# Performance work log

Hardware: AMD Instinct MI355X
Metric: run time of the kernel (lower is better)

Reference implementation:

```python
import jax, jax.numpy as jnp
import numpy as np
from jax import lax

PAD = 2
M1 = M2 = 12

def _gelu(v):
    return jax.nn.gelu(v, approximate=False)

def _spectral_conv(h, w1, w2):
    # h: [B,C,H,W] real; w1,w2: [C,C,M1,M2] complex64
    B, C, H, W = h.shape
    Wf = W // 2 + 1
    hft = jnp.fft.rfft2(h)  # [B,C,H,Wf] complex
    top = jnp.einsum('bixy,ioxy->boxy', hft[:, :, :M1, :M2], w1)
    bot = jnp.einsum('bixy,ioxy->boxy', hft[:, :, -M1:, :M2], w2)
    out_ft = jnp.zeros((B, C, H, Wf), jnp.complex64)
    out_ft = out_ft.at[:, :, :M1, :M2].set(top)
    out_ft = out_ft.at[:, :, -M1:, :M2].set(bot)
    return jnp.fft.irfft2(out_ft, s=(H, W))

def reference(x, grid, sentence_embeddings, fc0_w, fc0_b, sc_w1, sc_w2, wc_w, wc_b,
              pe1_w, pe1_b, pe2_w, pe2_b,
              sp_w1, sp_b1, sp_w2, sp_b2, sp_w3, sp_b3,
              xp_w1, xp_b1, xp_w2, xp_b2, xp_w3, xp_b3,
              pu_w1, pu_b1, pu_w2, pu_b2, pu_w3, pu_b3,
              fc1_w, fc1_b, fc2_w, fc2_b):
    B = x.shape[0]
    # sentence projection: Linear-ReLU-Linear-ReLU-Linear
    s = jax.nn.relu(sentence_embeddings @ sp_w1 + sp_b1)
    s = jax.nn.relu(s @ sp_w2 + sp_b2)
    sentence_emb = s @ sp_w3 + sp_b3  # [B,16]

    h = jnp.concatenate([x, grid], axis=-1) @ fc0_w + fc0_b  # [B,32,32,C]
    h = h.transpose(0, 3, 1, 2)  # [B,C,32,32]
    h = jnp.pad(h, ((0, 0), (0, 0), (0, PAD), (0, PAD)))  # [B,C,34,34]

    for i in range(4):
        w1 = sc_w1[i, ..., 0] + 1j * sc_w1[i, ..., 1]
        w2 = sc_w2[i, ..., 0] + 1j * sc_w2[i, ..., 1]
        x1 = _spectral_conv(h, w1, w2)
        x2 = jnp.einsum('bchw,oc->bohw', h, wc_w[i]) + wc_b[i][None, :, None, None]
        h = x1 + x2
        if i < 3:
            h = _gelu(h)  # dropout = identity (eval mode)

    # PatchEmbed: conv(k=8,s=4) -> gelu -> 1x1 conv
    p = lax.conv_general_dilated(h, pe1_w, (4, 4), 'VALID',
                                 dimension_numbers=('NCHW', 'OIHW', 'NCHW'))
    p = _gelu(p + pe1_b[None, :, None, None])  # [B,1,7,7]
    p = jnp.einsum('bchw,oc->bohw', p, pe2_w) + pe2_b[None, :, None, None]
    p = p.reshape(B, -1)  # [B,49]

    e = jax.nn.silu(p @ xp_w1 + xp_b1)
    e = jax.nn.silu(e @ xp_w2 + xp_b2)
    x_emb = e @ xp_w3 + xp_b3  # [B,16]

    emb = jnp.concatenate([x_emb, sentence_emb], axis=-1)  # [B,32]
    emb = jax.nn.silu(emb @ pu_w1 + pu_b1)
    emb = jax.nn.silu(emb @ pu_w2 + pu_b2)
    emb = (emb @ pu_w3 + pu_b3).reshape(B, 1, 34, 34)

    h = jnp.concatenate([h, emb], axis=1)  # [B,C+1,34,34]
    h = h[..., :-PAD, :-PAD]  # [B,C+1,32,32]
    h = h.transpose(0, 2, 3, 1)
    h = _gelu(h @ fc1_w + fc1_b)
    out = h @ fc2_w + fc2_b
    return out[..., None, :]  # [B,32,32,1,num_channels]

def setup_inputs() -> dict:
    key = jax.random.key(0)
    ks = iter(jax.random.split(key, 64))
    def rn(shape, scale=1.0):
        return jax.random.normal(next(ks), shape, jnp.float32) * scale
    C = 64
    inp = {
        'x': rn((256, 32, 32, 40)),
        'grid': jax.random.uniform(next(ks), (256, 32, 32, 2), jnp.float32),
        'sentence_embeddings': rn((256, 384)),
        'fc0_w': rn((42, C), 42 ** -0.5), 'fc0_b': jnp.zeros((C,), jnp.float32),
        'sc_w1': rn((4, C, C, M1, M2, 2), 1.0 / (C * C)),
        'sc_w2': rn((4, C, C, M1, M2, 2), 1.0 / (C * C)),
        'wc_w': rn((4, C, C), C ** -0.5), 'wc_b': jnp.zeros((4, C), jnp.float32),
        'pe1_w': rn((1, C, 8, 8), (C * 64) ** -0.5), 'pe1_b': jnp.zeros((1,), jnp.float32),
        'pe2_w': rn((1, 1)), 'pe2_b': jnp.zeros((1,), jnp.float32),
        'sp_w1': rn((384, 32), 384 ** -0.5), 'sp_b1': jnp.zeros((32,), jnp.float32),
        'sp_w2': rn((32, 32), 32 ** -0.5), 'sp_b2': jnp.zeros((32,), jnp.float32),
        'sp_w3': rn((32, 16), 32 ** -0.5), 'sp_b3': jnp.zeros((16,), jnp.float32),
        'xp_w1': rn((49, 32), 49 ** -0.5), 'xp_b1': jnp.zeros((32,), jnp.float32),
        'xp_w2': rn((32, 32), 32 ** -0.5), 'xp_b2': jnp.zeros((32,), jnp.float32),
        'xp_w3': rn((32, 16), 32 ** -0.5), 'xp_b3': jnp.zeros((16,), jnp.float32),
        'pu_w1': rn((32, 128), 32 ** -0.5), 'pu_b1': jnp.zeros((128,), jnp.float32),
        'pu_w2': rn((128, 256), 128 ** -0.5), 'pu_b2': jnp.zeros((256,), jnp.float32),
        'pu_w3': rn((256, 1156), 256 ** -0.5), 'pu_b3': jnp.zeros((1156,), jnp.float32),
        'fc1_w': rn((C + 1, 128), (C + 1) ** -0.5), 'fc1_b': jnp.zeros((128,), jnp.float32),
        'fc2_w': rn((128, 4), 128 ** -0.5), 'fc2_b': jnp.zeros((4,), jnp.float32),
    }
    return inp
```

## Files before the change

kernel.cpp:

```cpp
#include <hip/hip_runtime.h>
#include <hip/hip_bf16.h>
#include <math.h>

typedef __hip_bfloat16 bf16;
typedef __bf16 bfv8 __attribute__((ext_vector_type(8)));
typedef float fv4 __attribute__((ext_vector_type(4)));

__device__ __forceinline__ float bff(const bf16 x){ return __bfloat162float(x); }
__device__ __forceinline__ float gelu_f(float v){
    float x = v * 0.70710678118654752f;
    float ax = fabsf(x);
    float t = __builtin_amdgcn_rcpf(1.0f + 0.3275911f * ax);
    float y = t*(0.254829592f + t*(-0.284496736f + t*(1.421413741f +
              t*(-1.453152027f + t*1.061405429f))));
    float er = 1.0f - y * __expf(-ax*ax);
    er = (x < 0.f) ? -er : er;
    return 0.5f * v * (1.0f + er);
}
__device__ __forceinline__ float silu_f(float v){
    return v / (1.f + __expf(-v));
}
__device__ __forceinline__ float rdf(const void* p, size_t i, bool f32){
    return f32 ? ((const float*)p)[i] : __bfloat162float(((const bf16*)p)[i]);
}
__device__ __forceinline__ unsigned int packbf2(float a, float b){
    __hip_bfloat162 v;
    v.x = __float2bfloat16(a);
    v.y = __float2bfloat16(b);
    return *reinterpret_cast<unsigned int*>(&v);
}
__device__ __forceinline__ float2 unpackbf2(unsigned int u){
    __hip_bfloat162 v = *reinterpret_cast<__hip_bfloat162*>(&u);
    return make_float2(__bfloat162float(v.x), __bfloat162float(v.y));
}
__device__ __forceinline__ float us2f(unsigned short u){
    unsigned int x = ((unsigned int)u) << 16;
    return __uint_as_float(x);
}
__device__ __forceinline__ unsigned short f2us(float f){
    bf16 v = __float2bfloat16(f);
    return *reinterpret_cast<unsigned short*>(&v);
}


__global__ __launch_bounds__(256) void k_probe(const void* x, float* flag){
    __shared__ int wild;
    int t = threadIdx.x;
    if (t == 0) wild = 0;
    __syncthreads();
    const bf16* xb = (const bf16*)x;
    for (int i = t; i < 1024; i += 256){
        float v = bff(xb[i]);
        if (!(fabsf(v) < 1e10f)) wild = 1;
    }
    __syncthreads();
    if (t == 0) flag[0] = wild ? 1.f : 0.f;
}

__global__ __launch_bounds__(256) void k_tables(float* tabs, float* fwdimg,
                                                const void* __restrict__ fc0w,
                                                const void* __restrict__ fc0b,
                                                const float* __restrict__ flg){
    int t = threadIdx.x;
    const bool f32 = (flg[0] > 0.5f);
    unsigned int* gBT = (unsigned int*)(tabs + 2448);
    unsigned int* gW2 = (unsigned int*)(tabs + 3536);
    unsigned short* gB1 = (unsigned short*)fwdimg;
    unsigned short* gB2 = (unsigned short*)(fwdimg + 1024);
    unsigned short* gF  = (unsigned short*)(fwdimg + 3328);
    float* gFb = fwdimg + 5632;
    const float TWO_PI = 6.283185307179586f;
    for (int i = t; i < 4608; i += 256){
        int c = i / 72, k = i - c*72;
        float v = (k < 42) ? rdf(fc0w, (size_t)k*64 + c, f32) : 0.f;
        gF[i] = f2us(v);
    }
    if (t < 64) gFb[t] = rdf(fc0b, t, f32);
    for (int i = t; i < 2048; i += 256){
        int row = i >> 6, k = i & 63;
        float v = 0.f;
        if (row < 24 && k < 34){
            int kx = row >> 1, s = row & 1;
            int ph = (kx * k) % 34;
            float ang = TWO_PI * (float)ph / 34.0f;
            float sn, cs;
            sincosf(ang, &sn, &cs);
            v = (s == 0) ? cs : -sn;
        }
        gB1[i] = f2us(v);
    }
    for (int i = t; i < 4608; i += 256){
        int row = i / 96, kk = i - row*96;
        float v = 0.f;
        if (kk < 68){
            int kyi = row >> 1, s = row & 1;
            int y = kk >> 1, p = kk & 1;
            int ky = (kyi < 12) ? kyi : kyi + 10;
            int ph = (ky * y) % 34;
            float ang = TWO_PI * (float)ph / 34.0f;
            float sn, cs;
            sincosf(ang, &sn, &cs);
            float wr = cs, wi = -sn;
            v = (s == 0) ? ((p == 0) ? wr : -wi) : ((p == 0) ? wi : wr);
        }
        gB2[i] = f2us(v);
    }
    for (int i = t; i < 1088; i += 256){
        int n = i >> 4, kd = i & 15;
        int x = n >> 1, ri = n & 1;
        int kx = kd;
        float v0 = 0.f, v1 = 0.f;
        if (kx < 12){
            int ph = (kx * x) % 34;
            float ang = TWO_PI * (float)ph / 34.0f;
            float s, c;
            sincosf(ang, &s, &c);
            float ck = (kx == 0) ? 1.0f : 2.0f;
            float C = ck * c, S = ck * s;
            v0 = (ri == 0) ? C : S;
            v1 = (ri == 0) ? -S : C;
        }
        gBT[i] = packbf2(v0, v1);
    }
    for (int i = t; i < 1088; i += 256){
        int y = i >> 5, kd = i & 31;
        int kyi = kd;
        float v0 = 0.f, v1 = 0.f;
        if (kyi < 24){
            int ky = (kyi < 12) ? kyi : kyi + 10;
            int ph = (ky * y) % 34;
            float ang = TWO_PI * (float)ph / 34.0f;
            float s, c;
            sincosf(ang, &s, &c);
            v0 = c * (1.0f/1156.0f);
            v1 = -s * (1.0f/1156.0f);
        }
        gW2[i] = packbf2(v0, v1);
    }
}

__global__ __launch_bounds__(256) void k_fc0(const void* __restrict__ xin,
                                             const void* __restrict__ grd,
                                             const unsigned short* __restrict__ img,
                                             bf16* __restrict__ h,
                                             const float* __restrict__ flg){
    __shared__ unsigned short sA[128*72];
    const bool f32 = (flg[0] > 0.5f);
    int B = blockIdx.x;
    int b = (B >> 6)*8 + (B & 7);
    int u = (B >> 3) & 7;
    int t = threadIdx.x;
    unsigned int* sAw = (unsigned int*)sA;
    if (!f32){
        const unsigned int* xd = (const unsigned int*)xin;
        size_t base = ((size_t)b*1024 + u*128)*20;
        for (int i = t; i < 2560; i += 256){
            int p = i / 20, kd = i - p*20;
            sAw[p*36 + kd] = xd[base + i];
        }
        const unsigned int* gd = (const unsigned int*)grd;
        size_t gb = (size_t)b*1024 + (size_t)u*128;
        if (t < 128) sAw[t*36 + 20] = gd[gb + t];
    } else {
        const float* xf = (const float*)xin;
        size_t base = ((size_t)b*1024 + u*128)*40;
        for (int i = t; i < 2560; i += 256){
            int p = i / 20, kd = i - p*20;
            sAw[p*36 + kd] = packbf2(xf[base + 2*i], xf[base + 2*i + 1]);
        }
        const float* gf = (const float*)grd;
        size_t gb = ((size_t)b*1024 + u*128)*2;
        if (t < 128) sAw[t*36 + 20] = packbf2(gf[gb + 2*t], gf[gb + 2*t + 1]);
    }
    for (int i = t; i < 1920; i += 256){
        int p = i / 15, j = i - p*15;
        sAw[p*36 + 21 + j] = 0;
    }
    __syncthreads();
    int ln = t & 15, qd = (t & 63) >> 4, wv = t >> 6;
    const float* gbias = (const float*)(img + 4608);
    bfv8 bfr[4][2];
    #pragma unroll
    for (int nt = 0; nt < 4; ++nt)
        #pragma unroll
        for (int ks = 0; ks < 2; ++ks)
            bfr[nt][ks] = *reinterpret_cast<const bfv8*>(&img[(nt*16 + ln)*72 + ks*32 + qd*8]);
    bfv8 a_[2][2];
    #pragma unroll
    for (int mi = 0; mi < 2; ++mi){
        int mt = wv*2 + mi;
        a_[mi][0] = *reinterpret_cast<const bfv8*>(&sA[(mt*16 + ln)*72 + qd*8]);
        a_[mi][1] = *reinterpret_cast<const bfv8*>(&sA[(mt*16 + ln)*72 + 32 + qd*8]);
    }
    fv4 acc[2][4];
    #pragma unroll
    for (int mi = 0; mi < 2; ++mi)
        #pragma unroll
        for (int nt = 0; nt < 4; ++nt){
            fv4 a = (fv4){0.f,0.f,0.f,0.f};
            a = __builtin_amdgcn_mfma_f32_16x16x32_bf16(a_[mi][0], bfr[nt][0], a, 0, 0, 0);
            a = __builtin_amdgcn_mfma_f32_16x16x32_bf16(a_[mi][1], bfr[nt][1], a, 0, 0, 0);
            acc[mi][nt] = a;
        }
    __syncthreads();
    unsigned int* sCd = (unsigned int*)sA;
    {
        int c = t >> 2, r = t & 3;
        sCd[c*68 + r*17 + 16] = 0;
    }
    #pragma unroll
    for (int mi = 0; mi < 2; ++mi)
        #pragma unroll
        for (int nt = 0; nt < 4; ++nt){
            int c = nt*16 + ln;
            float bb = gbias[c];
            int pl = (wv*2 + mi)*16 + qd*4;
            int y = pl >> 5, x = pl & 31;
            int di = c*68 + y*17 + (x >> 1);
            sCd[di]     = packbf2(acc[mi][nt][0] + bb, acc[mi][nt][1] + bb);
            sCd[di + 1] = packbf2(acc[mi][nt][2] + bb, acc[mi][nt][3] + bb);
        }
    __syncthreads();
    unsigned int* hw = (unsigned int*)(h + (size_t)b*73984);
    for (int i = t; i < 4352; i += 256){
        int c = i / 68, d = i - c*68;
        hw[c*578 + u*68 + d] = sCd[i];
    }
    if (u == 7){
        for (int i = t; i < 2176; i += 256){
            int c = i / 34, d = i - c*34;
            hw[c*578 + 544 + d] = 0;
        }
    }
}

__global__ __launch_bounds__(256) void k_fwd(const bf16* __restrict__ h,
                                             unsigned int* __restrict__ hft,
                                             const unsigned short* __restrict__ fwdimg){
    __shared__ unsigned short lds[15360];
    unsigned short* sA1 = lds;
    unsigned short* sA2 = lds + 10368;
    unsigned int* sA1w = (unsigned int*)sA1;
    unsigned int* sA2w = (unsigned int*)sA2;
    const unsigned short* gB1 = fwdimg;
    const unsigned short* gB2 = fwdimg + 2048;
    int blk = blockIdx.x;
    int b = blk >> 4, c0 = (blk & 15) * 4;
    int t = threadIdx.x;
    const unsigned int* srcp = (const unsigned int*)(h + (size_t)b*73984 + (size_t)c0*1156);
    for (int i = t; i < 2312; i += 256){
        int c = i / 578; int rem = i - c*578;
        int y = rem / 17; int d = rem - y*17;
        sA1w[(c*34 + y)*36 + d] = srcp[i];
    }
    for (int i = t; i < 2040; i += 256){
        int r = i / 15, d = i - r*15;
        sA1w[r*36 + 17 + d] = 0;
    }
    for (int i = t; i < 288; i += 256){
        int r = 136 + i / 36, d = i - (i/36)*36;
        sA1w[r*36 + d] = 0;
    }
    for (int i = t; i < 672; i += 256){
        int r = i / 14, d = i - r*14;
        sA2w[r*52 + 34 + d] = 0;
    }
    __syncthreads();
    int ln = t & 15, qd = (t & 63) >> 4, wv = t >> 6;
    {
        int ntw = wv & 1;
        bfv8 b1f[2];
        #pragma unroll
        for (int ks = 0; ks < 2; ++ks)
            b1f[ks] = *reinterpret_cast<const bfv8*>(&gB1[(ntw*16 + ln)*64 + ks*32 + qd*8]);
        int col = ntw*16 + ln;
        int kx = col >> 1, s = col & 1;
        for (int mt = (wv >> 1); mt < 9; mt += 2){
            fv4 acc = (fv4){0.f,0.f,0.f,0.f};
            #pragma unroll
            for (int ks = 0; ks < 2; ++ks){
                bfv8 a = *reinterpret_cast<const bfv8*>(&sA1[(mt*16 + ln)*72 + ks*32 + qd*8]);
                acc = __builtin_amdgcn_mfma_f32_16x16x32_bf16(a, b1f[ks], acc, 0, 0, 0);
            }
            if (col < 24){
                #pragma unroll
                for (int rr = 0; rr < 4; ++rr){
                    int r = mt*16 + qd*4 + rr;
                    if (r < 136){
                        int c = r / 34, y = r - c*34;
                        sA2[(c*12 + kx)*104 + 2*y + s] = f2us(acc[rr]);
                    }
                }
            }
        }
    }
    __syncthreads();
    unsigned short* sC = sA1;
    for (int tau = wv; tau < 9; tau += 4){
        int mt = tau / 3, nt = tau - (tau/3)*3;
        fv4 acc = (fv4){0.f,0.f,0.f,0.f};
        #pragma unroll
        for (int ks = 0; ks < 3; ++ks){
            bfv8 a  = *reinterpret_cast<const bfv8*>(&sA2[(mt*16 + ln)*104 + ks*32 + qd*8]);
            bfv8 bb = *reinterpret_cast<const bfv8*>(&gB2[(nt*16 + ln)*96 + ks*32 + qd*8]);
            acc = __builtin_amdgcn_mfma_f32_16x16x32_bf16(a, bb, acc, 0, 0, 0);
        }
        int col = nt*16 + ln;
        int ky = col >> 1, s = col & 1;
        #pragma unroll
        for (int rr = 0; rr < 4; ++rr){
            int r = mt*16 + qd*4 + rr;
            int c = r / 12, kxx = r - c*12;
            sC[(ky*12 + kxx)*9 + s*4 + c] = f2us(acc[rr]);
        }
    }
    __syncthreads();
    unsigned int* dst = hft + ((size_t)(c0 >> 2)*256 + b)*1152;
    for (int d = t; d < 1152; d += 256){
        int m = d >> 2, j = d & 3;
        unsigned int lo = sC[m*9 + 2*j];
        unsigned int hi = sC[m*9 + 2*j + 1];
        dst[d] = lo | (hi << 16);
    }
}

__global__ __launch_bounds__(256) void k_mixm(const unsigned short* __restrict__ hft,
                                              const void* __restrict__ sc_w1,
                                              const void* __restrict__ sc_w2,
                                              unsigned int* __restrict__ mixed, int layer,
                                              const float* __restrict__ flg){
    __shared__ unsigned short sB[128*136];
    const bool f32 = (flg[0] > 0.5f);
    int B = blockIdx.x;
    int x8 = B & 7, w8 = B >> 3;
    int r4 = w8 & 3, g = w8 >> 2;
    int u = g*8 + x8;
    int mh = u & 1;
    int m  = (u >> 1)*4 + r4;
    int b0 = mh * 128;
    int t = threadIdx.x;
    int kyi = m / 12, kx = m - kyi*12;
    const void* w = (kyi < 12) ? sc_w1 : sc_w2;
    int r = (kyi < 12) ? kyi : kyi - 12;
    size_t wbase = (size_t)layer * 64*64*144*2;
    for (int idx = t; idx < 4096; idx += 256){
        int i = idx >> 6, o = idx & 63;
        size_t off = wbase + (((size_t)idx*12 + r)*12 + kx)*2;
        float wr = rdf(w, off, f32);
        float wi = rdf(w, off+1, f32);
        int kre = ((i >> 2) << 3) + (i & 3);
        sB[o*136 + kre]          = f2us(wr);
        sB[(o+64)*136 + kre]     = f2us(wi);
        sB[o*136 + kre + 4]      = f2us(-wi);
        sB[(o+64)*136 + kre + 4] = f2us(wr);
    }
    __syncthreads();
    int ln = t & 15, qd = (t & 63) >> 4, wv = t >> 6;
    bfv8 af[2][4];
    int arow = b0 + wv*32 + ln;
    #pragma unroll
    for (int tm = 0; tm < 2; ++tm)
        #pragma unroll
        for (int ks = 0; ks < 4; ++ks){
            int gg = ks*4 + qd;
            af[tm][ks] = *reinterpret_cast<const bfv8*>(
                hft + (((size_t)gg*256 + arow + tm*16)*288 + m)*8);
        }
    fv4 acc[2][8];
    #pragma unroll
    for (int tm=0;tm<2;++tm)
        #pragma unroll
        for (int tn=0;tn<8;++tn) acc[tm][tn] = (fv4){0.f,0.f,0.f,0.f};
    #pragma unroll
    for (int ks = 0; ks < 4; ++ks){
        bfv8 bfr[8];
        #pragma unroll
        for (int tn = 0; tn < 8; ++tn)
            bfr[tn] = *reinterpret_cast<const bfv8*>(&sB[(tn*16 + ln)*136 + ks*32 + qd*8]);
        #pragma unroll
        for (int tm = 0; tm < 2; ++tm)
            #pragma unroll
            for (int tn = 0; tn < 8; ++tn)
                acc[tm][tn] = __builtin_amdgcn_mfma_f32_16x16x32_bf16(af[tm][ks], bfr[tn], acc[tm][tn], 0, 0, 0);
    }
    __syncthreads();
    #pragma unroll
    for (int tm = 0; tm < 2; ++tm)
        #pragma unroll
        for (int tn = 0; tn < 8; ++tn)
            #pragma unroll
            for (int rr = 0; rr < 4; ++rr){
                int row = wv*32 + tm*16 + qd*4 + rr;
                int col = tn*16 + ln;
                sB[row*136 + col] = f2us(acc[tm][tn][rr]);
            }
    __syncthreads();
    for (int idx = t; idx < 8192; idx += 256){
        int row = idx >> 6, o = idx & 63;
        unsigned int pr = ((unsigned int)sB[row*136 + o]) |
                          (((unsigned int)sB[row*136 + o + 64]) << 16);
        mixed[((size_t)(b0 + row)*288 + m)*64 + o] = pr;
    }
}

__global__ __launch_bounds__(256) void k_wc(bf16* __restrict__ h,
                                            const void* __restrict__ wc_w,
                                            const void* __restrict__ wc_b,
                                            int layer,
                                            const float* __restrict__ flg){
    __shared__ unsigned short sA[240*72];
    __shared__ unsigned short sBT[64*72];
    __shared__ float sb[64];
    const bool f32 = (flg[0] > 0.5f);
    int blk = blockIdx.x;
    int b = blk & 255, u = blk >> 8;
    int px0 = u*240;
    int npx = 1156 - px0; if (npx > 240) npx = 240;
    int ndp = npx >> 1;
    int t = threadIdx.x;
    size_t wbase = (size_t)layer*4096;
    for (int i = t; i < 4096; i += 256){
        int o = i >> 6, c = i & 63;
        sBT[o*72 + c] = f2us(rdf(wc_w, wbase + i, f32));
    }
    if (t < 64) sb[t] = rdf(wc_b, layer*64 + t, f32);
    const unsigned int* srcd = (const unsigned int*)(h + (size_t)b*73984);
    for (int i = t; i < 7680; i += 256){
        int c = i / 120, dp = i - c*120;
        unsigned int v = (dp < ndp) ? srcd[c*578 + (px0 >> 1) + dp] : 0u;
        sA[(2*dp)*72 + c]     = (unsigned short)(v & 0xffff);
        sA[(2*dp + 1)*72 + c] = (unsigned short)(v >> 16);
    }
    __syncthreads();
    int ln = t & 15, qd = (t & 63) >> 4, wv = t >> 6;
    bfv8 bfr[4][2];
    #pragma unroll
    for (int nt = 0; nt < 4; ++nt)
        #pragma unroll
        for (int ks = 0; ks < 2; ++ks)
            bfr[nt][ks] = *reinterpret_cast<const bfv8*>(&sBT[(nt*16 + ln)*72 + ks*32 + qd*8]);
    bfv8 a_[4][2];
    #pragma unroll
    for (int mi = 0; mi < 4; ++mi){
        int mt = wv + mi*4;
        if (mt < 15){
            a_[mi][0] = *reinterpret_cast<const bfv8*>(&sA[(mt*16 + ln)*72 + qd*8]);
            a_[mi][1] = *reinterpret_cast<const bfv8*>(&sA[(mt*16 + ln)*72 + 32 + qd*8]);
        }
    }
    fv4 acc[4][4];
    #pragma unroll
    for (int mi = 0; mi < 4; ++mi){
        int mt = wv + mi*4;
        if (mt < 15){
            #pragma unroll
            for (int nt = 0; nt < 4; ++nt){
                fv4 a = (fv4){0.f,0.f,0.f,0.f};
                a = __builtin_amdgcn_mfma_f32_16x16x32_bf16(a_[mi][0], bfr[nt][0], a, 0, 0, 0);
                a = __builtin_amdgcn_mfma_f32_16x16x32_bf16(a_[mi][1], bfr[nt][1], a, 0, 0, 0);
                acc[mi][nt] = a;
            }
        }
    }
    __syncthreads();
    unsigned int* sCd = (unsigned int*)sA;
    #pragma unroll
    for (int mi = 0; mi < 4; ++mi){
        int mt = wv + mi*4;
        if (mt < 15){
            #pragma unroll
            for (int nt = 0; nt < 4; ++nt){
                int o = nt*16 + ln;
                float bb = sb[o];
                int p0 = mt*16 + qd*4;
                sCd[o*120 + (p0 >> 1)]     = packbf2(acc[mi][nt][0] + bb, acc[mi][nt][1] + bb);
                sCd[o*120 + (p0 >> 1) + 1] = packbf2(acc[mi][nt][2] + bb, acc[mi][nt][3] + bb);
            }
        }
    }
    __syncthreads();
    unsigned int* dstd = (unsigned int*)(h + (size_t)b*73984);
    for (int i = t; i < 7680; i += 256){
        int o = i / 120, dp = i - o*120;
        if (dp < ndp) dstd[o*578 + (px0 >> 1) + dp] = sCd[o*120 + dp];
    }
}

__global__ __launch_bounds__(256, 5) void k_invm(const unsigned int* __restrict__ mixed,
                                              const float* __restrict__ tabs,
                                              bf16* __restrict__ hio, int layer){
    __shared__ unsigned short lds[15072];
    unsigned short* sA   = lds;
    unsigned short* sG16 = lds + 3840;
    unsigned int* ldsw   = (unsigned int*)lds;
    unsigned int* sGd    = ldsw + 1920;
    float* rawf          = (float*)(ldsw + 1920);
    int B = blockIdx.x;
    int x8 = B & 7, s4 = (B >> 3) & 3, z = B >> 5;
    int b  = (z >> 2)*8 + x8;
    int o0 = ((z & 3)*4 + s4)*4;
    int t = threadIdx.x;
    const unsigned short* gBT16 = (const unsigned short*)(tabs + 2448);
    const unsigned short* gW216 = (const unsigned short*)(tabs + 3536);
    const unsigned int* msrc = mixed + (size_t)b*18432 + o0;
    for (int i = t; i < 1152; i += 256){
        int m = i >> 2, ch = i & 3;
        int kyi = m / 12, kx = m - kyi*12;
        ((unsigned int*)sA)[(ch*24 + kyi)*20 + kx] = msrc[(size_t)m*64 + ch];
    }
    for (int i = t; i < 384; i += 256)
        ((unsigned int*)sA)[(i >> 2)*20 + 12 + (i & 3)] = 0;
    for (int i = t; i < 1088; i += 256){
        int r = i >> 3;
        int ch = r / 34, x = r - ch*34;
        sGd[(ch*36 + x)*36 + 24 + (i & 7)] = 0;
    }
    __syncthreads();
    int ln = t & 15, qd = (t & 63) >> 4, wv = t >> 6;
    for (int tau = wv; tau < 30; tau += 4){
        int mt = tau / 5, nt = tau - mt*5;
        bfv8 a  = *reinterpret_cast<const bfv8*>(&sA[(mt*16 + ln)*40 + qd*8]);
        bfv8 bb = *reinterpret_cast<const bfv8*>(&gBT16[(nt*16 + ln)*32 + qd*8]);
        fv4 acc = (fv4){0.f,0.f,0.f,0.f};
        acc = __builtin_amdgcn_mfma_f32_16x16x32_bf16(a, bb, acc, 0, 0, 0);
        int col = nt*16 + ln;
        if (col < 68){
            int x = col >> 1, ri = col & 1;
            #pragma unroll
            for (int rr = 0; rr < 4; ++rr){
                int row = mt*16 + qd*4 + rr;
                int ch = row / 24, kyi = row - ch*24;
                sG16[(ch*36 + x)*72 + 2*kyi + ri] = f2us(acc[rr]);
            }
        }
    }
    __syncthreads();
    int ch = wv;
    fv4 accB[3][3];
    #pragma unroll
    for (int mt = 0; mt < 3; ++mt){
        bfv8 a0 = *reinterpret_cast<const bfv8*>(&gW216[(mt*16 + ln)*64 + qd*8]);
        bfv8 a1 = *reinterpret_cast<const bfv8*>(&gW216[(mt*16 + ln)*64 + 32 + qd*8]);
        #pragma unroll
        for (int nt = 0; nt < 3; ++nt){
            bfv8 b0 = *reinterpret_cast<const bfv8*>(&sG16[(ch*36 + nt*16 + ln)*72 + qd*8]);
            bfv8 b1 = *reinterpret_cast<const bfv8*>(&sG16[(ch*36 + nt*16 + ln)*72 + 32 + qd*8]);
            fv4 acc = (fv4){0.f,0.f,0.f,0.f};
            acc = __builtin_amdgcn_mfma_f32_16x16x32_bf16(a0, b0, acc, 0, 0, 0);
            acc = __builtin_amdgcn_mfma_f32_16x16x32_bf16(a1, b1, acc, 0, 0, 0);
            accB[mt][nt] = acc;
        }
    }
    __syncthreads();
    #pragma unroll
    for (int mt = 0; mt < 3; ++mt)
        #pragma unroll
        for (int nt = 0; nt < 3; ++nt){
            int x = nt*16 + ln;
            if (x < 34){
                #pragma unroll
                for (int rr = 0; rr < 4; ++rr){
                    int y = mt*16 + qd*4 + rr;
                    if (y < 34) rawf[ch*1156 + y*34 + x] = accB[mt][nt][rr];
                }
            }
        }
    __syncthreads();
    const unsigned int* hsrc = (const unsigned int*)(hio + (size_t)b*73984 + (size_t)o0*1156);
    unsigned int* hdst = (unsigned int*)(hio + (size_t)b*73984 + (size_t)o0*1156);
    for (int i = t; i < 2312; i += 256){
        float2 rv = *reinterpret_cast<const float2*>(&rawf[2*i]);
        float2 hv = unpackbf2(hsrc[i]);
        float v0 = rv.x + hv.x, v1 = rv.y + hv.y;
        if (layer < 3){ v0 = gelu_f(v0); v1 = gelu_f(v1); }
        hdst[i] = packbf2(v0, v1);
    }
}

__global__ __launch_bounds__(256) void k_pe(const bf16* __restrict__ h,
                                            const void* __restrict__ pw,
                                            const void* __restrict__ pb,
                                            const void* __restrict__ p2w,
                                            const void* __restrict__ p2b,
                                            float* __restrict__ p49,
                                            const float* __restrict__ flg){
    __shared__ float red[256];
    const bool f32 = (flg[0] > 0.5f);
    int bid = blockIdx.x;
    int b = bid / 49, r = bid - b*49;
    int py = r / 7, px = r - py*7;
    int t = threadIdx.x;
    const bf16* hb = h + (size_t)b*73984 + (py*4)*34 + px*4;
    float partial = 0.f;
    for (int tt = t; tt < 4096; tt += 256){
        int c = tt >> 6, k = tt & 63, ky = k >> 3, kx = k & 7;
        partial += bff(hb[(size_t)c*1156 + ky*34 + kx]) * rdf(pw, tt, f32);
    }
    red[t] = partial;
    __syncthreads();
    for (int s = 128; s > 0; s >>= 1){
        if (t < s) red[t] += red[t + s];
        __syncthreads();
    }
    if (t == 0){
        float v = red[0] + rdf(pb, 0, f32);
        v = gelu_f(v);
        p49[bid] = v * rdf(p2w, 0, f32) + rdf(p2b, 0, f32);
    }
}

__global__ __launch_bounds__(256) void k_sent(const void* __restrict__ se,
                                             const void* __restrict__ w1, const void* __restrict__ b1,
                                             const void* __restrict__ w2, const void* __restrict__ b2,
                                             const void* __restrict__ w3, const void* __restrict__ b3,
                                             float* __restrict__ outv,
                                             const float* __restrict__ flg){
    __shared__ float sse[384];
    __shared__ float red[256];
    __shared__ float s1[32], s2[32];
    const bool f32 = (flg[0] > 0.5f);
    int b = blockIdx.x, t = threadIdx.x;
    for (int i = t; i < 384; i += 256) sse[i] = rdf(se, (size_t)b*384 + i, f32);
    __syncthreads();
    {
        int o = t & 31, g = t >> 5;
        float acc = 0.f;
        #pragma unroll 4
        for (int k = g*48; k < g*48 + 48; ++k)
            acc += sse[k] * rdf(w1, (size_t)k*32 + o, f32);
        red[t] = acc;
    }
    __syncthreads();
    if (t < 32){
        float a = rdf(b1, t, f32);
        #pragma unroll
        for (int g = 0; g < 8; ++g) a += red[g*32 + t];
        s1[t] = fmaxf(a, 0.f);
    }
    __syncthreads();
    if (t < 32){
        float acc = rdf(b2, t, f32);
        for (int k = 0; k < 32; ++k) acc += s1[k] * rdf(w2, k*32 + t, f32);
        s2[t] = fmaxf(acc, 0.f);
    }
    __syncthreads();
    if (t < 16){
        float acc = rdf(b3, t, f32);
        for (int k = 0; k < 32; ++k) acc += s2[k] * rdf(w3, k*16 + t, f32);
        outv[b*16 + t] = acc;
    }
}

__global__ __launch_bounds__(256) void k_xp(const float* __restrict__ p49,
                                           const void* __restrict__ w1, const void* __restrict__ b1,
                                           const void* __restrict__ w2, const void* __restrict__ b2,
                                           const void* __restrict__ w3, const void* __restrict__ b3,
                                           float* __restrict__ outv,
                                           const float* __restrict__ flg){
    __shared__ float sp[49];
    __shared__ float red[256];
    __shared__ float s1[32], s2[32];
    const bool f32 = (flg[0] > 0.5f);
    int b = blockIdx.x, t = threadIdx.x;
    if (t < 49) sp[t] = p49[b*49 + t];
    __syncthreads();
    {
        int o = t & 31, g = t >> 5;
        float acc = 0.f;
        for (int k = g; k < 49; k += 8)
            acc += sp[k] * rdf(w1, (size_t)k*32 + o, f32);
        red[t] = acc;
    }
    __syncthreads();
    if (t < 32){
        float a = rdf(b1, t, f32);
        #pragma unroll
        for (int g = 0; g < 8; ++g) a += red[g*32 + t];
        s1[t] = silu_f(a);
    }
    __syncthreads();
    if (t < 32){
        float acc = rdf(b2, t, f32);
        for (int k = 0; k < 32; ++k) acc += s1[k] * rdf(w2, k*32 + t, f32);
        s2[t] = silu_f(acc);
    }
    __syncthreads();
    if (t < 16){
        float acc = rdf(b3, t, f32);
        for (int k = 0; k < 32; ++k) acc += s2[k] * rdf(w3, k*16 + t, f32);
        outv[b*16 + t] = acc;
    }
}

__global__ __launch_bounds__(256) void k_puA(const float* __restrict__ xemb,
                                             const float* __restrict__ semb,
                                             const void* __restrict__ w1, const void* __restrict__ b1,
                                             const void* __restrict__ w2, const void* __restrict__ b2,
                                             float* __restrict__ h2buf,
                                             const float* __restrict__ flg){
    __shared__ float ein[32];
    __shared__ float h1[128];
    const bool f32 = (flg[0] > 0.5f);
    int b = blockIdx.x, t = threadIdx.x;
    if (t < 16) ein[t] = xemb[b*16 + t];
    else if (t < 32) ein[t] = semb[b*16 + (t - 16)];
    __syncthreads();
    if (t < 128){
        float acc = rdf(b1, t, f32);
        for (int k = 0; k < 32; ++k) acc += ein[k] * rdf(w1, k*128 + t, f32);
        h1[t] = silu_f(acc);
    }
    __syncthreads();
    {
        float acc = rdf(b2, t, f32);
        for (int k = 0; k < 128; ++k) acc += h1[k] * rdf(w2, k*256 + t, f32);
        h2buf[(size_t)b*256 + t] = silu_f(acc);
    }
}

__global__ __launch_bounds__(256) void k_puB(const float* __restrict__ h2buf,
                                             const void* __restrict__ w3, const void* __restrict__ b3,
                                             float* __restrict__ emb,
                                             const float* __restrict__ flg){
    __shared__ float sh2[256];
    const bool f32 = (flg[0] > 0.5f);
    int blk = blockIdx.x;
    int b = blk & 255, nc = blk >> 8;
    int t = threadIdx.x;
    sh2[t] = h2buf[(size_t)b*256 + t];
    __syncthreads();
    int e = nc*232 + t;
    if (t < 232 && e < 1156){
        float acc = rdf(b3, e, f32);
        if (f32){
            const float* wp = (const float*)w3 + e;
            #pragma unroll 4
            for (int k = 0; k < 256; ++k) acc += sh2[k] * wp[(size_t)k*1156];
        } else {
            const bf16* wp = (const bf16*)w3 + e;
            #pragma unroll 4
            for (int k = 0; k < 256; ++k) acc += sh2[k] * bff(wp[(size_t)k*1156]);
        }
        emb[(size_t)b*1156 + e] = acc;
    }
}

__global__ __launch_bounds__(256, 3) void k_final(const bf16* __restrict__ h,
                                                  const float* __restrict__ emb,
                                                  const void* __restrict__ w1, const void* __restrict__ b1,
                                                  const void* __restrict__ w2, const void* __restrict__ b2,
                                                  void* __restrict__ out,
                                                  const float* __restrict__ flg){
    __shared__ unsigned short sw1t[128*72];
    __shared__ unsigned short sw2t[16*136];
    __shared__ float sw1e[128];
    __shared__ float sb1[128];
    __shared__ float sb2[4];
    __shared__ unsigned short spx[64*66];
    __shared__ float sembp[64];
    __shared__ unsigned short sh2[128*66];
    const bool f32 = (flg[0] > 0.5f);
    int blk = blockIdx.x;
    int b = blk >> 1, half = blk & 1;
    int t = threadIdx.x;
    for (int i = t; i < 8320; i += 256){
        int c = i >> 7, j = i & 127;
        float v = rdf(w1, i, f32);
        if (c < 64) sw1t[j*72 + c] = f2us(v);
        else sw1e[j] = v;
    }
    if (t < 128) sb1[t] = rdf(b1, t, f32);
    for (int i = t; i < 2176; i += 256){
        int n = i / 136, j = i - n*136;
        float v = (n < 4 && j < 128) ? rdf(w2, j*4 + n, f32) : 0.f;
        sw2t[i] = f2us(v);
    }
    if (t < 4) sb2[t] = rdf(b2, t, f32);
    __syncthreads();
    int ln = t & 15, qd = (t & 63) >> 4, wv = t >> 6;
    bfv8 bw1[8][2];
    #pragma unroll
    for (int tn = 0; tn < 8; ++tn)
        #pragma unroll
        for (int ks = 0; ks < 2; ++ks)
            bw1[tn][ks] = *reinterpret_cast<const bfv8*>(&sw1t[(tn*16 + ln)*72 + ks*32 + qd*8]);
    bfv8 bw2[4];
    #pragma unroll
    for (int ks = 0; ks < 4; ++ks)
        bw2[ks] = *reinterpret_cast<const bfv8*>(&sw2t[ln*136 + ks*32 + qd*8]);
    const bf16* hb = h + (size_t)b*73984;
    const float* eb = emb + (size_t)b*1156;
    for (int it = 0; it < 8; ++it){
        int y0 = half*16 + it*2;
        __syncthreads();
        for (int e = t; e < 2048; e += 256){
            int c = e >> 5, d = e & 31;
            int px = d*2;
            int y = y0 + (px >> 5), x = px & 31;
            float v0 = bff(hb[(size_t)c*1156 + y*34 + x]);
            int px1 = px + 1;
            int y1 = y0 + (px1 >> 5), x1 = px1 & 31;
            float v1 = bff(hb[(size_t)c*1156 + y1*34 + x1]);
            ((unsigned int*)spx)[c*33 + d] = packbf2(v0, v1);
        }
        if (t < 64){
            int y = y0 + (t >> 5), x = t & 31;
            sembp[t] = eb[y*34 + x];
        }
        __syncthreads();
        fv4 acc[8];
        #pragma unroll
        for (int tn = 0; tn < 8; ++tn) acc[tn] = (fv4){0.f,0.f,0.f,0.f};
        #pragma unroll
        for (int ks = 0; ks < 2; ++ks){
            union { bfv8 v; unsigned short s[8]; } af;
            #pragma unroll
            for (int j = 0; j < 8; ++j)
                af.s[j] = spx[(ks*32 + qd*8 + j)*66 + wv*16 + ln];
            #pragma unroll
            for (int tn = 0; tn < 8; ++tn)
                acc[tn] = __builtin_amdgcn_mfma_f32_16x16x32_bf16(af.v, bw1[tn][ks], acc[tn], 0, 0, 0);
        }
        float ev[4];
        #pragma unroll
        for (int rr = 0; rr < 4; ++rr) ev[rr] = sembp[wv*16 + qd*4 + rr];
        #pragma unroll
        for (int tn = 0; tn < 8; ++tn){
            int col = tn*16 + ln;
            float we = sw1e[col];
            float bb1 = sb1[col];
            #pragma unroll
            for (int rr = 0; rr < 4; ++rr){
                float v = acc[tn][rr] + ev[rr]*we + bb1;
                sh2[col*66 + wv*16 + qd*4 + rr] = f2us(gelu_f(v));
            }
        }
        __syncthreads();
        fv4 a2 = (fv4){0.f,0.f,0.f,0.f};
        #pragma unroll
        for (int ks = 0; ks < 4; ++ks){
            union { bfv8 v; unsigned short s[8]; } af;
            #pragma unroll
            for (int j = 0; j < 8; ++j)
                af.s[j] = sh2[(ks*32 + qd*8 + j)*66 + wv*16 + ln];
            a2 = __builtin_amdgcn_mfma_f32_16x16x32_bf16(af.v, bw2[ks], a2, 0, 0, 0);
        }
        if (ln < 4){
            float bb2 = sb2[ln];
            #pragma unroll
            for (int rr = 0; rr < 4; ++rr){
                int pxl = wv*16 + qd*4 + rr;
                int y = y0 + (pxl >> 5), x = pxl & 31;
                size_t o = ((size_t)(b*32 + y)*32 + x)*4 + ln;
                float v = a2[rr] + bb2;
                if (f32) ((float*)out)[o] = v;
                else     ((bf16*)out)[o] = __float2bfloat16(v);
            }
        }
    }
}

extern "C" void kernel_launch(void* const* d_in, const int* in_sizes, int n_in,
                              void* d_out, int out_size, void* d_ws, size_t ws_size,
                              hipStream_t stream) {
    (void)in_sizes; (void)n_in; (void)out_size; (void)ws_size;
    const void* x     = d_in[0];
    const void* grd   = d_in[1];
    const void* se    = d_in[2];
    const void* fc0_w = d_in[3];
    const void* fc0_b = d_in[4];
    const void* sc_w1 = d_in[5];
    const void* sc_w2 = d_in[6];
    const void* wc_w  = d_in[7];
    const void* wc_b  = d_in[8];
    const void* pe1_w = d_in[9];
    const void* pe1_b = d_in[10];
    const void* pe2_w = d_in[11];
    const void* pe2_b = d_in[12];
    const void* sp_w1 = d_in[13];
    const void* sp_b1 = d_in[14];
    const void* sp_w2 = d_in[15];
    const void* sp_b2 = d_in[16];
    const void* sp_w3 = d_in[17];
    const void* sp_b3 = d_in[18];
    const void* xp_w1 = d_in[19];
    const void* xp_b1 = d_in[20];
    const void* xp_w2 = d_in[21];
    const void* xp_b2 = d_in[22];
    const void* xp_w3 = d_in[23];
    const void* xp_b3 = d_in[24];
    const void* pu_w1 = d_in[25];
    const void* pu_b1 = d_in[26];
    const void* pu_w2 = d_in[27];
    const void* pu_b2 = d_in[28];
    const void* pu_w3 = d_in[29];
    const void* pu_b3 = d_in[30];
    const void* fc1_w = d_in[31];
    const void* fc1_b = d_in[32];
    const void* fc2_w = d_in[33];
    const void* fc2_b = d_in[34];

    float* ws    = (float*)d_ws;
    bf16*  hA    = (bf16*)ws;
    unsigned int* hft   = (unsigned int*)(ws + 9469952);
    unsigned int* mixed = (unsigned int*)(ws + 14188544);
    float* tabs  = ws + 18907136;
    float* p49   = ws + 18912032;
    float* semb  = ws + 18924576;
    float* xemb  = ws + 18928672;
    float* emb   = ws + 18932768;
    float* flag  = ws + 19228704;
    float* h2buf = (float*)hft;
    float* fwdimg = emb;

    k_probe<<<1, 256, 0, stream>>>(x, flag);
    k_tables<<<1, 256, 0, stream>>>(tabs, fwdimg, fc0_w, fc0_b, flag);
    k_fc0<<<2048, 256, 0, stream>>>(x, grd, (const unsigned short*)(fwdimg + 3328), hA, flag);

    for (int l = 0; l < 4; ++l){
        k_fwd<<<4096, 256, 0, stream>>>(hA, hft, (const unsigned short*)fwdimg);
        k_mixm<<<576, 256, 0, stream>>>((const unsigned short*)hft, sc_w1, sc_w2, mixed, l, flag);
        k_wc <<<1280, 256, 0, stream>>>(hA, wc_w, wc_b, l, flag);
        k_invm<<<4096, 256, 0, stream>>>(mixed, tabs, hA, l);
    }

    k_pe  <<<256*49, 256, 0, stream>>>(hA, pe1_w, pe1_b, pe2_w, pe2_b, p49, flag);
    k_sent<<<256, 256, 0, stream>>>(se, sp_w1, sp_b1, sp_w2, sp_b2, sp_w3, sp_b3, semb, flag);
    k_xp  <<<256, 256, 0, stream>>>(p49, xp_w1, xp_b1, xp_w2, xp_b2, xp_w3, xp_b3, xemb, flag);
    k_puA <<<256, 256, 0, stream>>>(xemb, semb, pu_w1, pu_b1, pu_w2, pu_b2, h2buf, flag);
    k_puB <<<1280, 256, 0, stream>>>(h2buf, pu_w3, pu_b3, emb, flag);
    k_final<<<512, 256, 0, stream>>>(hA, emb, fc1_w, fc1_b, fc2_w, fc2_b, d_out, flag);
}
```

Measured before the change: 1.002 ms.

## Restructure patch-embed conv to stage a row band in LDS and reuse it across outputs

The patch-embed kernel now launches one block per (batch, output row) instead of one per output pixel. Each block copies the 8-row input band for all 64 channels into shared memory once, keeps the conv weights in registers, and computes all 7 outputs of the row from that staged band. The shared-memory tree reduction is replaced by wavefront shuffles plus a small cross-wave sum. This is meant to remove the heavily redundant global reads of overlapping 8x8 windows and the sync-heavy reduction. In exchange each block uses about 35KB of LDS, which limits occupancy.

```diff
diff --git a/kernel.cpp b/kernel.cpp
--- a/kernel.cpp
+++ b/kernel.cpp
@@ -584,28 +584,47 @@
                                             const void* __restrict__ p2b,
                                             float* __restrict__ p49,
                                             const float* __restrict__ flg){
-    __shared__ float red[256];
+    __shared__ unsigned short sh16[64*274];
+    __shared__ float wred[28];
     const bool f32 = (flg[0] > 0.5f);
-    int bid = blockIdx.x;
-    int b = bid / 49, r = bid - b*49;
-    int py = r / 7, px = r - py*7;
+    int B = blockIdx.x;
+    int x8 = B & 7, w8 = B >> 3;
+    int py = w8 % 7, z = w8 / 7;
+    int b = z*8 + x8;
     int t = threadIdx.x;
-    const bf16* hb = h + (size_t)b*73984 + (py*4)*34 + px*4;
-    float partial = 0.f;
-    for (int tt = t; tt < 4096; tt += 256){
-        int c = tt >> 6, k = tt & 63, ky = k >> 3, kx = k & 7;
-        partial += bff(hb[(size_t)c*1156 + ky*34 + kx]) * rdf(pw, tt, f32);
-    }
-    red[t] = partial;
-    __syncthreads();
-    for (int s = 128; s > 0; s >>= 1){
-        if (t < s) red[t] += red[t + s];
-        __syncthreads();
-    }
-    if (t == 0){
-        float v = red[0] + rdf(pb, 0, f32);
-        v = gelu_f(v);
-        p49[bid] = v * rdf(p2w, 0, f32) + rdf(p2b, 0, f32);
+    unsigned int* shd = (unsigned int*)sh16;
+    const unsigned int* srcd = (const unsigned int*)(h + (size_t)b*73984);
+    for (int i = t; i < 8704; i += 256){
+        int c = i / 136, d = i - c*136;
+        shd[c*137 + d] = srcd[c*578 + py*68 + d];
+    }
+    int c = t & 63, q = t >> 6;
+    float wreg[16];
+    int aoff[16];
+    #pragma unroll
+    for (int j = 0; j < 16; ++j){
+        int k = q*16 + j, ky = k >> 3, kx = k & 7;
+        wreg[j] = rdf(pw, (size_t)c*64 + k, f32);
+        aoff[j] = c*274 + ky*34 + kx;
+    }
+    __syncthreads();
+    int wv = t >> 6, ln = t & 63;
+    #pragma unroll
+    for (int px = 0; px < 7; ++px){
+        float s = 0.f;
+        #pragma unroll
+        for (int j = 0; j < 16; ++j)
+            s += us2f(sh16[aoff[j] + px*4]) * wreg[j];
+        #pragma unroll
+        for (int sh = 32; sh > 0; sh >>= 1)
+            s += __shfl_down(s, sh, 64);
+        if (ln == 0) wred[wv*7 + px] = s;
+    }
+    __syncthreads();
+    if (t < 7){
+        float v = wred[t] + wred[7 + t] + wred[14 + t] + wred[21 + t];
+        v = gelu_f(v + rdf(pb, 0, f32));
+        p49[b*49 + py*7 + t] = v * rdf(p2w, 0, f32) + rdf(p2b, 0, f32);
     }
 }
 
@@ -924,7 +943,7 @@
         k_invm<<<4096, 256, 0, stream>>>(mixed, tabs, hA, l);
     }
 
-    k_pe  <<<256*49, 256, 0, stream>>>(hA, pe1_w, pe1_b, pe2_w, pe2_b, p49, flag);
+    k_pe  <<<1792, 256, 0, stream>>>(hA, pe1_w, pe1_b, pe2_w, pe2_b, p49, flag);
     k_sent<<<256, 256, 0, stream>>>(se, sp_w1, sp_b1, sp_w2, sp_b2, sp_w3, sp_b3, semb, flag);
     k_xp  <<<256, 256, 0, stream>>>(p49, xp_w1, xp_b1, xp_w2, xp_b2, xp_w3, xp_b3, xemb, flag);
     k_puA <<<256, 256, 0, stream>>>(xemb, semb, pu_w1, pu_b1, pu_w2, pu_b2, h2buf, flag);
```

Result: no change. 1.010 ms (+0.8%).
